# Kernel tuning notes

Measured on AMD Instinct MI355X. Metric: run time of the kernel, lower is better.

The kernel has to match this reference:

```python
import jax, jax.numpy as jnp
import numpy as np

N_NODES = 50000


def gcn_conv(x, W, b, edge_index, n):
    # PyG GCNConv(add_self_loops=False): h = x @ W; out[c] = sum_e norm_e * h[row_e]
    # with norm_e = deg(row)^-1/2 * deg(col)^-1/2, deg = in-degree on col.
    h = x @ W  # [N, out]
    row, col = edge_index[0], edge_index[1]
    deg = jax.ops.segment_sum(jnp.ones(row.shape, h.dtype), col, num_segments=n)
    dis = jnp.where(deg > 0, jax.lax.rsqrt(jnp.where(deg > 0, deg, 1.0)), 0.0)
    norm = dis[row] * dis[col]  # [E]
    msg = h[row] * norm[:, None]  # [E, out]
    out = jax.ops.segment_sum(msg, col, num_segments=n)
    return out + b


def setup_inputs() -> dict:
    key = jax.random.key(0)
    ks = jax.random.split(key, 12)
    N, F, H0, H1, H2, C = N_NODES, 512, 256, 128, 128, 40
    E1, E2 = 800000, 1600000
    s = 0.05
    return {
        "x": jax.random.normal(ks[0], (N, F), jnp.float32),
        "edge_index": jax.random.randint(ks[1], (2, E1), 0, N, jnp.int32),
        "edge_index2": jax.random.randint(ks[2], (2, E2), 0, N, jnp.int32),
        "W_lin1": jax.random.normal(ks[3], (F, H0), jnp.float32) * s,
        "b_lin1": jnp.zeros((H0,), jnp.float32),
        "W_c1": jax.random.normal(ks[4], (H0, H1), jnp.float32) * s,
        "b_c1": jnp.zeros((H1,), jnp.float32),
        "W_c2": jax.random.normal(ks[5], (2 * H1, H2), jnp.float32) * s,
        "b_c2": jnp.zeros((H2,), jnp.float32),
        "W_lin2": jax.random.normal(ks[6], (H0 + 2 * H1 + 2 * H2, C), jnp.float32) * s,
        "b_lin2": jnp.zeros((C,), jnp.float32),
    }


def reference(x, edge_index, edge_index2, W_lin1, b_lin1, W_c1, b_c1, W_c2, b_c2, W_lin2, b_lin2):
    n = x.shape[0]
    h = jax.nn.relu(x @ W_lin1 + b_lin1)  # [N, H0]
    first_hop_h = gcn_conv(h, W_c1, b_c1, edge_index, n)
    second_hop_h = gcn_conv(h, W_c1, b_c1, edge_index2, n)
    R1 = jnp.concatenate([first_hop_h, second_hop_h], axis=1)  # [N, 2*H1]
    first_hop_h2 = gcn_conv(R1, W_c2, b_c2, edge_index, n)
    second_hop_h2 = gcn_conv(R1, W_c2, b_c2, edge_index2, n)
    R2 = jnp.concatenate([first_hop_h2, second_hop_h2], axis=1)  # [N, 2*H2]
    final_h = jnp.concatenate([h, R1, R2], axis=1)  # [N, H0+2H1+2H2]
    # dropout treated as identity (eval / deterministic reference)
    logits = final_h @ W_lin2 + b_lin2
    return jax.nn.log_softmax(logits, axis=1)
```

## Files before the change

kernel.cpp:

```cpp
#include <hip/hip_runtime.h>
#include <hip/hip_bf16.h>
#include <stdint.h>

typedef __attribute__((ext_vector_type(8))) short bf16x8;
typedef __attribute__((ext_vector_type(8))) unsigned short ushort8v;
typedef __attribute__((ext_vector_type(4))) float f32x4;
typedef __attribute__((ext_vector_type(2))) float f32x2;
typedef __attribute__((ext_vector_type(4))) unsigned int u32x4;
typedef unsigned long long ull;

__device__ __forceinline__ void load_lds16(const void* g, void* l){
  __builtin_amdgcn_global_load_lds((const __attribute__((address_space(1))) void*)g,
                                   (__attribute__((address_space(3))) void*)l, 16, 0, 0);
}

__device__ __forceinline__ float bf2f(unsigned int u){
  union { unsigned int i; float f; } x; x.i = u << 16; return x.f;
}
__device__ __forceinline__ unsigned short f2bf(float f){
  __hip_bfloat16 h = __float2bfloat16(f);
  unsigned short u;
  __builtin_memcpy(&u, &h, 2);
  return u;
}

__global__ void wtrans4_kernel(const float* __restrict__ W1, unsigned short* __restrict__ Wt1,
                               const float* __restrict__ Wc1, unsigned short* __restrict__ Wtc1,
                               const float* __restrict__ Wc2, unsigned short* __restrict__ Wtc2,
                               const float* __restrict__ Wf, unsigned short* __restrict__ Wtf,
                               int NB, int cap1r, int cap2r, int* __restrict__ bcur,
                               unsigned* __restrict__ Tz0, unsigned* __restrict__ Tz1){
  int idx = blockIdx.x*256 + threadIdx.x;
  if (idx >= 245760){
    int i = idx - 245760;
    if (i < NB) bcur[i] = i*cap1r;
    else if (i < 2*NB) bcur[i] = NB*cap1r + (i - NB)*cap2r;
    else if (i < 2*NB + 32) Tz0[i - 2*NB] = 0u;
    else if (i < 2*NB + 64) Tz1[i - 2*NB - 32] = 0u;
    return;
  }
  const float* W; unsigned short* Wt; int K, N;
  if (idx < 131072){ W = W1; Wt = Wt1; K = 512; N = 256; }
  else if (idx < 163840){ idx -= 131072; W = Wc1; Wt = Wtc1; K = 256; N = 128; }
  else if (idx < 196608){ idx -= 163840; W = Wc2; Wt = Wtc2; K = 256; N = 128; }
  else { idx -= 196608; W = Wf; Wt = Wtf; K = 768; N = 40; }
  int nn = idx / K, kk = idx - nn*K;
  float v = (nn < N) ? W[(size_t)kk*N + nn] : 0.f;
  Wt[idx] = f2bf(v);
}


#define PCH 4096

__global__ __launch_bounds__(256) void partA_kernel(
    const int* __restrict__ ei1, int E1, const int* __restrict__ ei2, int E2,
    int* __restrict__ bcur, unsigned* __restrict__ staging, int NB)
{
  const int set = blockIdx.y;
  const int* __restrict__ ei = set ? ei2 : ei1;
  const int E = set ? E2 : E1;
  int* __restrict__ cur = bcur + set*NB;
  __shared__ int hist[400];
  __shared__ int resv[400];
  const int tid = threadIdx.x;
  const int base = blockIdx.x * PCH;
  if (base >= E) return;
  for (int b = tid; b < NB; b += 256) hist[b] = 0;
  __syncthreads();

  if (base + PCH <= E){
    const int t0 = base + tid*16;
    int4 c[4], r[4];
    #pragma unroll
    for (int j = 0; j < 4; ++j) c[j] = *(const int4*)(ei + E + t0 + j*4);
    #pragma unroll
    for (int j = 0; j < 4; ++j) r[j] = *(const int4*)(ei + t0 + j*4);
    #pragma unroll
    for (int j = 0; j < 4; ++j){
      atomicAdd(&hist[c[j].x >> 7], 1); atomicAdd(&hist[c[j].y >> 7], 1);
      atomicAdd(&hist[c[j].z >> 7], 1); atomicAdd(&hist[c[j].w >> 7], 1);
    }
    __syncthreads();
    for (int b = tid; b < NB; b += 256){
      int hc = hist[b];
      resv[b] = hc ? atomicAdd(&cur[b], hc) : 0;
      hist[b] = 0;
    }
    __syncthreads();
    #pragma unroll
    for (int j = 0; j < 4; ++j){
      int cc, rr, b, s;
      cc = c[j].x; rr = r[j].x; b = cc >> 7;
      s = resv[b] + atomicAdd(&hist[b], 1);
      staging[s] = ((unsigned)rr << 7) | (unsigned)(cc & 127);
      cc = c[j].y; rr = r[j].y; b = cc >> 7;
      s = resv[b] + atomicAdd(&hist[b], 1);
      staging[s] = ((unsigned)rr << 7) | (unsigned)(cc & 127);
      cc = c[j].z; rr = r[j].z; b = cc >> 7;
      s = resv[b] + atomicAdd(&hist[b], 1);
      staging[s] = ((unsigned)rr << 7) | (unsigned)(cc & 127);
      cc = c[j].w; rr = r[j].w; b = cc >> 7;
      s = resv[b] + atomicAdd(&hist[b], 1);
      staging[s] = ((unsigned)rr << 7) | (unsigned)(cc & 127);
    }
  } else {
    for (int i = 0; i < PCH/256; ++i){
      int e = base + i*256 + tid;
      if (e < E) atomicAdd(&hist[ei[E + e] >> 7], 1);
    }
    __syncthreads();
    for (int b = tid; b < NB; b += 256){
      int hc = hist[b];
      resv[b] = hc ? atomicAdd(&cur[b], hc) : 0;
      hist[b] = 0;
    }
    __syncthreads();
    for (int i = 0; i < PCH/256; ++i){
      int e = base + i*256 + tid;
      if (e < E){
        int c = ei[E + e], r = ei[e];
        int b = c >> 7;
        int s = resv[b] + atomicAdd(&hist[b], 1);
        staging[s] = ((unsigned)r << 7) | (unsigned)(c & 127);
      }
    }
  }
}

__global__ __launch_bounds__(256) void degB_kernel(
    const unsigned* __restrict__ staging, const int* __restrict__ bcur,
    int* __restrict__ deg1, int* __restrict__ deg2,
    float* __restrict__ dis1, float* __restrict__ dis2,
    int NB, int n, int cap1r, int cap2r)
{
  const int set = blockIdx.y;
  int* __restrict__ deg = set ? deg2 : deg1;
  float* __restrict__ dis = set ? dis2 : dis1;
  const int b = blockIdx.x;
  const int nodebase = b << 7;
  const int nn = min(128, n - nodebase);
  if (nn <= 0) return;
  __shared__ int cnt[128];
  const int tid = threadIdx.x;
  if (tid < 128) cnt[tid] = 0;
  __syncthreads();
  const int s0 = set ? (NB*cap1r + b*cap2r) : (b*cap1r);
  const int s1 = bcur[set*NB + b];
  for (int i = s0 + tid; i < s1; i += 256)
    atomicAdd(&cnt[staging[i] & 127], 1);
  __syncthreads();
  if (tid < nn){
    int c = cnt[tid];
    deg[nodebase + tid] = c;
    dis[nodebase + tid] = (c > 0) ? (1.0f/sqrtf((float)c)) : 0.f;
  }
}

__global__ void scan1_kernel(const int* __restrict__ deg1, const int* __restrict__ deg2,
                             int* __restrict__ off1, int* __restrict__ off2,
                             int* __restrict__ bsum, int n){
  __shared__ int s[1024];
  int set = blockIdx.y;
  const int* deg = set ? deg2 : deg1;
  int* off = set ? off2 : off1;
  int tid = threadIdx.x;
  int i = blockIdx.x*1024 + tid;
  int v = (i < n) ? ((deg[i] + 7) & ~7) : 0;
  s[tid] = v;
  __syncthreads();
  for (int o = 1; o < 1024; o <<= 1){
    int t = (tid >= o) ? s[tid - o] : 0;
    __syncthreads();
    s[tid] += t;
    __syncthreads();
  }
  if (i < n) off[i] = s[tid];
  if (tid == 1023) bsum[set*64 + blockIdx.x] = s[1023];
}

__global__ void scan2_kernel(const int* __restrict__ bsum, int* __restrict__ bbase,
                             int nch, int* __restrict__ off1, int* __restrict__ off2, int n){
  int set = threadIdx.x;
  if (set < 2){
    int run = 0;
    for (int j = 0; j < nch; ++j){ bbase[set*64 + j] = run; run += bsum[set*64 + j]; }
    (set ? off2 : off1)[n] = run;
  }
}

__global__ void scan3_kernel(const int* __restrict__ deg1, const int* __restrict__ deg2,
                             int* __restrict__ off1, int* __restrict__ off2,
                             const int* __restrict__ bbase, int n){
  int set = blockIdx.y;
  const int* deg = set ? deg2 : deg1;
  int* off = set ? off2 : off1;
  int i = blockIdx.x*1024 + threadIdx.x;
  if (i < n){
    int e = off[i] + bbase[set*64 + blockIdx.x];
    off[i] = e - ((deg[i] + 7) & ~7);
  }
}

__global__ __launch_bounds__(256) void partB_kernel(
    const unsigned* __restrict__ staging, const int* __restrict__ bcur,
    const int* __restrict__ off1, const int* __restrict__ off2,
    unsigned* __restrict__ csr1, unsigned* __restrict__ csr2,
    int NB, int n, unsigned padrow, int cap1r, int cap2r)
{
  const int set = blockIdx.y;
  const int* __restrict__ off = set ? off2 : off1;
  unsigned* __restrict__ csr = set ? csr2 : csr1;
  const int b = blockIdx.x;
  const int nodebase = b << 7;
  const int nn = min(128, n - nodebase);
  if (nn <= 0) return;
  __shared__ int offv[129];
  __shared__ int curl[128];
  const int tid = threadIdx.x;
  if (tid <= nn) offv[tid] = off[nodebase + tid];
  if (tid < 128) curl[tid] = 0;
  __syncthreads();
  const int s0 = set ? (NB*cap1r + b*cap2r) : (b*cap1r);
  const int s1 = bcur[set*NB + b];
  for (int i = s0 + tid; i < s1; i += 256){
    unsigned v = staging[i];
    int cl = v & 127;
    int p = offv[cl] + atomicAdd(&curl[cl], 1);
    csr[p] = v >> 7;
  }
  __syncthreads();
  for (int c = tid; c < nn; c += 256){
    int p1 = offv[c+1];
    for (int p = offv[c] + curl[c]; p < p1; ++p) csr[p] = padrow;
  }
  if (b == 0 && tid < 64) csr[off[n] + tid] = padrow;
}

__global__ __launch_bounds__(256) void conv_kernel(
    const int* __restrict__ off1, const unsigned* __restrict__ csr1, const float* __restrict__ dis1,
    const int* __restrict__ off2, const unsigned* __restrict__ csr2, const float* __restrict__ dis2,
    const unsigned char* __restrict__ Tbase,
    const float* __restrict__ bias, unsigned short* __restrict__ outR,
    int n, int ntab)
{
  const int set = blockIdx.y;
  const int* __restrict__ off = set ? off2 : off1;
  const float* __restrict__ dis = set ? dis2 : dis1;
  const unsigned* __restrict__ csrq = set ? csr2 : csr1;
  const int col_ofs = set ? 128 : 0;
  const unsigned* __restrict__ tab =
      (const unsigned*)(Tbase + (size_t)set * ntab * 128);

  int wv = blockIdx.x*4 + (threadIdx.x >> 6);
  if (wv >= n) return;
  const int l = threadIdx.x & 63;
  const int half = l >> 5, lf = l & 31;
  const int s = off[wv], e = off[wv+1];
  const int nb = (e - s) >> 3;
  const unsigned* cp = csrq + s + half*4;

  float ax = 0.f, ay = 0.f, az = 0.f, aw = 0.f;

  if (nb > 0){
    u32x4 qa, qb;
    unsigned va0, va1, va2, va3, vb0, vb1, vb2, vb3;

#define LQ(q, B) q = __builtin_nontemporal_load((const u32x4*)(cp + (B)*8));
#define GATH(v, q) \
    v##0 = tab[(size_t)q.x * 32 + lf]; \
    v##1 = tab[(size_t)q.y * 32 + lf]; \
    v##2 = tab[(size_t)q.z * 32 + lf]; \
    v##3 = tab[(size_t)q.w * 32 + lf];
#define FMA1(v) { \
    f32x2 lo = __builtin_amdgcn_cvt_pk_f32_fp8((int)v, false); \
    f32x2 hi = __builtin_amdgcn_cvt_pk_f32_fp8((int)v, true);  \
    ax += lo.x; ay += lo.y; az += hi.x; aw += hi.y; }
#define FMAB(v) { FMA1(v##0) FMA1(v##1) FMA1(v##2) FMA1(v##3) }

    LQ(qa, 0)
    GATH(va, qa)
    LQ(qb, 1)
    int b = 0;
    while (b + 2 <= nb){
      LQ(qa, b + 2)
      GATH(vb, qb)
      FMAB(va)
      LQ(qb, b + 3)
      GATH(va, qa)
      FMAB(vb)
      b += 2;
    }
    if (b < nb) FMAB(va)
#undef LQ
#undef GATH
#undef FMA1
#undef FMAB
  }

  ax += __shfl_xor(ax, 32, 64);
  ay += __shfl_xor(ay, 32, 64);
  az += __shfl_xor(az, 32, 64);
  aw += __shfl_xor(aw, 32, 64);

  if (half == 0){
    const float dc = dis[wv];
    float b0 = bias[lf*4 + 0], b1 = bias[lf*4 + 1];
    float b2 = bias[lf*4 + 2], b3 = bias[lf*4 + 3];
    ull ov = (ull)((unsigned)f2bf(fmaf(dc, ax, b0)) | ((unsigned)f2bf(fmaf(dc, ay, b1)) << 16))
           | ((ull)((unsigned)f2bf(fmaf(dc, az, b2)) | ((unsigned)f2bf(fmaf(dc, aw, b3)) << 16)) << 32);
    __builtin_nontemporal_store(ov, (ull*)&outR[(size_t)wv*256 + col_ofs + lf*4]);
  }
}

template<int FM, int FN, int WGM, int WGN, int EPI, bool AF32>
__global__ __launch_bounds__(WGM*WGN*64, (WGM*WGN*64) == 512 ? 4 : 2) void gemm_kernel(
    const unsigned short* __restrict__ A0, const float* __restrict__ Af,
    const unsigned short* __restrict__ A1, const unsigned short* __restrict__ A2,
    const unsigned short* __restrict__ Bt, const float* __restrict__ bias,
    void* __restrict__ Cout, int M, int K, int lda, int ldc,
    const float* __restrict__ d1, const float* __restrict__ d2, int ntab)
{
  constexpr int THREADS = WGM*WGN*64;
  constexpr int BM = WGM*FM*16;
  constexpr int BN = WGN*FN*16;
  constexpr int BK = 32;
  constexpr int AJ = (BM*BK/8)/THREADS;
  constexpr int BJ = (BN*BK/8)/THREADS;
  static_assert(BM == 128, "staging assumes BM==128");
  __shared__ unsigned short As[BM][BK];
  __shared__ unsigned short Bs[BN][BK];
  const int tid = threadIdx.x;
  const int w = tid >> 6, l = tid & 63;
  const int wr = w / WGN, wc = w % WGN;
  const int m0 = blockIdx.x*BM, n0 = blockIdx.y*BN;
  f32x4 acc[FM][FN] = {};
  const int nsteps = K / BK;
  for (int s = 0; s < nsteps; ++s){
    const int k0 = s*BK;
    const unsigned short* Asrc = A0;
    int kin = k0;
    if constexpr (EPI == 2){
      int slab = k0 >> 8;
      Asrc = (slab == 0) ? A0 : ((slab == 1) ? A1 : A2);
      kin = k0 & 255;
    }
    __syncthreads();
    if constexpr (AF32){
      #pragma unroll
      for (int j = 0; j < AJ; ++j){
        int idx = j*THREADS + tid;
        int row = idx >> 2, kq = idx & 3;
        int rg = m0 + row; rg = (rg < M) ? rg : (M - 1);
        const float* src = Af + (size_t)rg*lda + kin + kq*8;
        float4 a = *(const float4*)src;
        float4 b2 = *(const float4*)(src + 4);
        ushort8v u;
        u[0] = f2bf(a.x);  u[1] = f2bf(a.y);  u[2] = f2bf(a.z);  u[3] = f2bf(a.w);
        u[4] = f2bf(b2.x); u[5] = f2bf(b2.y); u[6] = f2bf(b2.z); u[7] = f2bf(b2.w);
        *(ushort8v*)((char*)&As[0][0] + (size_t)idx*16) = u;
      }
    } else {
      #pragma unroll
      for (int j = 0; j < AJ; ++j){
        int idx = j*THREADS + tid;
        int row = idx >> 2, kq = idx & 3;
        int rg = m0 + row; rg = (rg < M) ? rg : (M - 1);
        load_lds16(Asrc + (size_t)rg*lda + kin + kq*8,
                   ((char*)&As[0][0]) + (size_t)(j*THREADS + w*64)*16);
      }
    }
    #pragma unroll
    for (int j = 0; j < BJ; ++j){
      int idx = j*THREADS + tid;
      int row = idx >> 2, kq = idx & 3;
      load_lds16(Bt + (size_t)(n0 + row)*K + k0 + kq*8,
                 ((char*)&Bs[0][0]) + (size_t)(j*THREADS + w*64)*16);
    }
    __syncthreads();
    bf16x8 af[FM], bfr[FN];
    const int kofs = (l >> 4)*8, l16 = l & 15;
    #pragma unroll
    for (int mi = 0; mi < FM; ++mi)
      af[mi] = *(const bf16x8*)&As[wr*FM*16 + mi*16 + l16][kofs];
    #pragma unroll
    for (int ni = 0; ni < FN; ++ni)
      bfr[ni] = *(const bf16x8*)&Bs[wc*FN*16 + ni*16 + l16][kofs];
    #pragma unroll
    for (int mi = 0; mi < FM; ++mi)
      #pragma unroll
      for (int ni = 0; ni < FN; ++ni)
        acc[mi][ni] = __builtin_amdgcn_mfma_f32_16x16x32_bf16(af[mi], bfr[ni], acc[mi][ni], 0, 0, 0);
  }
  const int lg = l >> 4, lc = l & 15;
  if constexpr (EPI == 2){
    float* O = (float*)Cout;
    #pragma unroll
    for (int mi = 0; mi < FM; ++mi){
      #pragma unroll
      for (int i = 0; i < 4; ++i){
        int row = m0 + wr*FM*16 + mi*16 + lg*4 + i;
        float v[FN];
        float mx = -1e30f;
        #pragma unroll
        for (int ni = 0; ni < FN; ++ni){
          int col = ni*16 + lc;
          v[ni] = acc[mi][ni][i] + ((col < 40) ? bias[col] : 0.f);
          if (col < 40) mx = fmaxf(mx, v[ni]);
        }
        #pragma unroll
        for (int d = 1; d < 16; d <<= 1) mx = fmaxf(mx, __shfl_xor(mx, d, 64));
        float se = 0.f;
        #pragma unroll
        for (int ni = 0; ni < FN; ++ni){
          int col = ni*16 + lc;
          if (col < 40) se += expf(v[ni] - mx);
        }
        #pragma unroll
        for (int d = 1; d < 16; d <<= 1) se += __shfl_xor(se, d, 64);
        float lse = logf(se);
        if (row < M){
          #pragma unroll
          for (int ni = 0; ni < FN; ++ni){
            int col = ni*16 + lc;
            if (col < 40) O[(size_t)row*40 + col] = v[ni] - mx - lse;
          }
        }
      }
    }
  } else if constexpr (EPI == 4){
    unsigned char* T = (unsigned char*)Cout;
    #pragma unroll
    for (int mi = 0; mi < FM; ++mi){
      #pragma unroll
      for (int i = 0; i < 4; ++i){
        int row = m0 + wr*FM*16 + mi*16 + lg*4 + i;
        if (row >= M) continue;
        float s1 = d1[row], s2 = d2[row];
        #pragma unroll
        for (int ni = 0; ni < FN; ++ni){
          int col = n0 + wc*FN*16 + ni*16 + lc;
          float vv = acc[mi][ni][i];
          unsigned p1 = (unsigned)__builtin_amdgcn_cvt_pk_fp8_f32(vv*s1, vv*s1, 0, false);
          unsigned p2 = (unsigned)__builtin_amdgcn_cvt_pk_fp8_f32(vv*s2, vv*s2, 0, false);
          T[(size_t)row*128 + col] = (unsigned char)(p1 & 0xff);
          T[((size_t)ntab + row)*128 + col] = (unsigned char)(p2 & 0xff);
        }
      }
    }
  } else {
    unsigned short* C = (unsigned short*)Cout;
    #pragma unroll
    for (int mi = 0; mi < FM; ++mi){
      #pragma unroll
      for (int i = 0; i < 4; ++i){
        int row = m0 + wr*FM*16 + mi*16 + lg*4 + i;
        if (row >= M) continue;
        #pragma unroll
        for (int ni = 0; ni < FN; ++ni){
          int col = n0 + wc*FN*16 + ni*16 + lc;
          float vv = acc[mi][ni][i];
          if constexpr (EPI == 1){ vv += bias[col]; vv = fmaxf(vv, 0.f); }
          C[(size_t)row*ldc + col] = f2bf(vv);
        }
      }
    }
  }
}

extern "C" void kernel_launch(void* const* d_in, const int* in_sizes, int n_in,
                              void* d_out, int out_size, void* d_ws, size_t ws_size,
                              hipStream_t stream)
{
  (void)n_in; (void)out_size;
  const float* x      = (const float*)d_in[0];
  const int*   ei1    = (const int*)d_in[1];
  const int*   ei2    = (const int*)d_in[2];
  const float* W_lin1 = (const float*)d_in[3];
  const float* b_lin1 = (const float*)d_in[4];
  const float* W_c1   = (const float*)d_in[5];
  const float* b_c1   = (const float*)d_in[6];
  const float* W_c2   = (const float*)d_in[7];
  const float* b_c2   = (const float*)d_in[8];
  const float* W_lin2 = (const float*)d_in[9];
  const float* b_lin2 = (const float*)d_in[10];

  const int N  = in_sizes[0] / 512;
  const int E1 = in_sizes[1] / 2;
  const int E2 = in_sizes[2] / 2;
  const int ntab = N + 1;
  const int NB = (N + 127) >> 7;
  const int cap1r = (((E1 + NB - 1)/NB + 768) + 63) & ~63;
  const int cap2r = (((E2 + NB - 1)/NB + 1536) + 63) & ~63;

  char* base = (char*)d_ws;
  size_t off = 0;
  auto alloc = [&](size_t bytes) -> char* {
    off = (off + 255) & ~(size_t)255;
    char* r = base + off;
    off += bytes;
    return r;
  };
  const size_t cap1 = (size_t)E1 + 8*(size_t)N + 64;
  const size_t cap2 = (size_t)E2 + 8*(size_t)N + 64;

  unsigned short* h    = (unsigned short*)alloc((size_t)N*256*2);
  unsigned char*  T    = (unsigned char*)alloc((size_t)2*ntab*128);
  unsigned short* R1   = (unsigned short*)alloc((size_t)N*256*2);
  unsigned short* R2   = (unsigned short*)alloc((size_t)N*256*2);
  unsigned short* Wt1  = (unsigned short*)alloc((size_t)256*512*2);
  unsigned short* Wtc1 = (unsigned short*)alloc((size_t)128*256*2);
  unsigned short* Wtc2 = (unsigned short*)alloc((size_t)128*256*2);
  unsigned short* Wtf  = (unsigned short*)alloc((size_t)64*768*2);
  int* degblk = (int*)alloc((size_t)2*N*4);
  int* deg1 = degblk, *deg2 = degblk + N;
  float* dis1 = (float*)alloc((size_t)N*4);
  float* dis2 = (float*)alloc((size_t)N*4);
  int* off1 = (int*)alloc((size_t)(N+1)*4);
  int* off2 = (int*)alloc((size_t)(N+1)*4);
  int* bsum  = (int*)alloc(128*4);
  int* bbase = (int*)alloc(128*4);
  int* bcur  = (int*)alloc((size_t)2*NB*4);
  unsigned* csr1 = (unsigned*)alloc(cap1*4);
  unsigned* csr2 = (unsigned*)alloc(cap2*4);
  unsigned* staging = (unsigned*)alloc((size_t)NB*((size_t)cap1r + cap2r)*4);
  if (off > ws_size) return;

  int mt = (N + 127)/128;
  int cb = (N + 3)/4;

  wtrans4_kernel<<<(245760 + 2*NB + 64 + 255)/256, 256, 0, stream>>>(
      W_lin1, Wt1, W_c1, Wtc1, W_c2, Wtc2, W_lin2, Wtf,
      NB, cap1r, cap2r, bcur,
      (unsigned*)(T + (size_t)N*128), (unsigned*)(T + ((size_t)ntab + N)*128));
  gemm_kernel<4,4,2,4,1,true><<<dim3(mt, 1), 512, 0, stream>>>(
      nullptr, x, nullptr, nullptr, Wt1, b_lin1, h, N, 512, 512, 256, nullptr, nullptr, 0);

  partA_kernel<<<dim3((E2 + PCH - 1)/PCH, 2), 256, 0, stream>>>(ei1, E1, ei2, E2, bcur, staging, NB);
  degB_kernel<<<dim3(NB, 2), 256, 0, stream>>>(staging, bcur, deg1, deg2, dis1, dis2,
                                               NB, N, cap1r, cap2r);
  int nch = (N + 1023)/1024;
  scan1_kernel<<<dim3(nch, 2), 1024, 0, stream>>>(deg1, deg2, off1, off2, bsum, N);
  scan2_kernel<<<1, 64, 0, stream>>>(bsum, bbase, nch, off1, off2, N);
  scan3_kernel<<<dim3(nch, 2), 1024, 0, stream>>>(deg1, deg2, off1, off2, bbase, N);
  partB_kernel<<<dim3(NB, 2), 256, 0, stream>>>(staging, bcur, off1, off2, csr1, csr2,
                                                NB, N, (unsigned)N, cap1r, cap2r);

  gemm_kernel<4,4,2,2,4,false><<<dim3(mt, 1), 256, 0, stream>>>(
      h, nullptr, nullptr, nullptr, Wtc1, nullptr, T, N, 256, 256, 0, dis1, dis2, ntab);
  conv_kernel<<<dim3(cb, 2), 256, 0, stream>>>(off1, csr1, dis1, off2, csr2, dis2,
                                               T, b_c1, R1, N, ntab);
  gemm_kernel<4,4,2,2,4,false><<<dim3(mt, 1), 256, 0, stream>>>(
      R1, nullptr, nullptr, nullptr, Wtc2, nullptr, T, N, 256, 256, 0, dis1, dis2, ntab);
  conv_kernel<<<dim3(cb, 2), 256, 0, stream>>>(off1, csr1, dis1, off2, csr2, dis2,
                                               T, b_c2, R2, N, ntab);
  gemm_kernel<2,4,4,1,2,false><<<dim3(mt, 1), 256, 0, stream>>>(
      h, nullptr, R1, R2, Wtf, b_lin2, d_out, N, 768, 256, 40, nullptr, nullptr, 0);
}
```

Baseline: 261.9 us.

## Process eight consecutive nodes per wavefront in conv kernel with continuous edge stream

Each wavefront in the GCN aggregation kernel now covers a run of eight consecutive destination nodes. It streams their padded CSR edge batches as one continuous pipeline and emits each node's result at its segment boundary. This keeps the software-pipelined gather busy across node boundaries and cuts the prologue cost per node and the idle waves for low-degree nodes. In exchange it adds boundary-check shuffles inside the hot loop and launches fewer waves, which lowers occupancy.

Measured after the change: 248.2 us. 5.2% less time.

```diff
diff --git a/kernel.cpp b/kernel.cpp
--- a/kernel.cpp
+++ b/kernel.cpp
@@ -48,7 +48,6 @@
   float v = (nn < N) ? W[(size_t)kk*N + nn] : 0.f;
   Wt[idx] = f2bf(v);
 }
-
 
 #define PCH 4096
 
@@ -236,6 +235,7 @@
   if (b == 0 && tid < 64) csr[off[n] + tid] = padrow;
 }
 
+#define KN 8
 __global__ __launch_bounds__(256) void conv_kernel(
     const int* __restrict__ off1, const unsigned* __restrict__ csr1, const float* __restrict__ dis1,
     const int* __restrict__ off2, const unsigned* __restrict__ csr2, const float* __restrict__ dis2,
@@ -251,17 +251,46 @@
   const unsigned* __restrict__ tab =
       (const unsigned*)(Tbase + (size_t)set * ntab * 128);
 
-  int wv = blockIdx.x*4 + (threadIdx.x >> 6);
-  if (wv >= n) return;
+  const int wv0 = (blockIdx.x*4 + (threadIdx.x >> 6)) * KN;
+  if (wv0 >= n) return;
+  const int wend = min(n, wv0 + KN);
   const int l = threadIdx.x & 63;
   const int half = l >> 5, lf = l & 31;
-  const int s = off[wv], e = off[wv+1];
-  const int nb = (e - s) >> 3;
-  const unsigned* cp = csrq + s + half*4;
+  const float b0 = bias[lf*4 + 0], b1 = bias[lf*4 + 1];
+  const float b2 = bias[lf*4 + 2], b3 = bias[lf*4 + 3];
+
+  const int offs = off[wv0 + min(l, wend - wv0)];
+  const int cstart = __shfl(offs, 0, 64);
+  const int pend   = __shfl(offs, wend - wv0, 64);
+  int node = wv0;
+  int nxt  = __shfl(offs, min(1, wend - wv0), 64);
 
   float ax = 0.f, ay = 0.f, az = 0.f, aw = 0.f;
 
-  if (nb > 0){
+#define EMIT_NODE { \
+    float rx = ax + __shfl_xor(ax, 32, 64); \
+    float ry = ay + __shfl_xor(ay, 32, 64); \
+    float rz = az + __shfl_xor(az, 32, 64); \
+    float rw = aw + __shfl_xor(aw, 32, 64); \
+    if (half == 0){ \
+      const float dc = dis[node]; \
+      ull ov = (ull)((unsigned)f2bf(fmaf(dc, rx, b0)) | ((unsigned)f2bf(fmaf(dc, ry, b1)) << 16)) \
+             | ((ull)((unsigned)f2bf(fmaf(dc, rz, b2)) | ((unsigned)f2bf(fmaf(dc, rw, b3)) << 16)) << 32); \
+      __builtin_nontemporal_store(ov, (ull*)&outR[(size_t)node*256 + col_ofs + lf*4]); \
+    } \
+    ax = ay = az = aw = 0.f; }
+#define DRAIN(CUR) \
+    while (node < wend && (CUR) == nxt){ \
+      EMIT_NODE \
+      ++node; \
+      nxt = __shfl(offs, min(node + 1 - wv0, KN), 64); \
+    }
+
+  DRAIN(cstart)
+
+  const int nbat = (pend - cstart) >> 3;
+  if (nbat > 0){
+    const unsigned* cp = csrq + cstart + half*4;
     u32x4 qa, qb;
     unsigned va0, va1, va2, va3, vb0, vb1, vb2, vb3;
 
@@ -281,35 +310,29 @@
     GATH(va, qa)
     LQ(qb, 1)
     int b = 0;
-    while (b + 2 <= nb){
+    while (b + 2 <= nbat){
       LQ(qa, b + 2)
       GATH(vb, qb)
       FMAB(va)
+      DRAIN(cstart + (b + 1)*8)
       LQ(qb, b + 3)
       GATH(va, qa)
       FMAB(vb)
+      DRAIN(cstart + (b + 2)*8)
       b += 2;
     }
-    if (b < nb) FMAB(va)
+    if (b < nbat){
+      FMAB(va)
+      DRAIN(cstart + nbat*8)
+    }
 #undef LQ
 #undef GATH
 #undef FMA1
 #undef FMAB
   }
-
-  ax += __shfl_xor(ax, 32, 64);
-  ay += __shfl_xor(ay, 32, 64);
-  az += __shfl_xor(az, 32, 64);
-  aw += __shfl_xor(aw, 32, 64);
-
-  if (half == 0){
-    const float dc = dis[wv];
-    float b0 = bias[lf*4 + 0], b1 = bias[lf*4 + 1];
-    float b2 = bias[lf*4 + 2], b3 = bias[lf*4 + 3];
-    ull ov = (ull)((unsigned)f2bf(fmaf(dc, ax, b0)) | ((unsigned)f2bf(fmaf(dc, ay, b1)) << 16))
-           | ((ull)((unsigned)f2bf(fmaf(dc, az, b2)) | ((unsigned)f2bf(fmaf(dc, aw, b3)) << 16)) << 32);
-    __builtin_nontemporal_store(ov, (ull*)&outR[(size_t)wv*256 + col_ofs + lf*4]);
-  }
+  while (node < wend){ EMIT_NODE ++node; }
+#undef EMIT_NODE
+#undef DRAIN
 }
 
 template<int FM, int FN, int WGM, int WGN, int EPI, bool AF32>
@@ -526,7 +549,8 @@
   if (off > ws_size) return;
 
   int mt = (N + 127)/128;
-  int cb = (N + 3)/4;
+  int nwv = (N + KN - 1)/KN;
+  int cb = (nwv + 3)/4;
 
   wtrans4_kernel<<<(245760 + 2*NB + 64 + 255)/256, 256, 0, stream>>>(
       W_lin1, Wt1, W_c1, Wtc1, W_c2, Wtc2, W_lin2, Wtf,
```
